# Kernel tuning notes

Hardware: AMD Instinct MI355X
Metric: run time of the kernel (lower is better)

## Reference

```python
import jax, jax.numpy as jnp
import numpy as np

N, E, G = 100_000, 1_600_000, 64
NODE_DIM, EDGE_DIM = 64, 16
H, C = 4, 16            # heads, per-head channels (hidden_dim=64)
HID = H * C             # 64
OUT = 128
NEG_SLOPE = 0.2


def _gatv2(x, src, dst, ea, Wl, bl, Wr, br, We, att, bias, n):
    """One GATv2Conv layer (PyG semantics, concat=True). src/dst include self-loops."""
    xl = (x @ Wl + bl).reshape(-1, H, C)   # [n,H,C] source transform
    xr = (x @ Wr + br).reshape(-1, H, C)   # [n,H,C] target transform
    e = (ea @ We).reshape(-1, H, C)        # [E2,H,C] edge transform (no bias)
    m = jax.nn.leaky_relu(xl[src] + xr[dst] + e, NEG_SLOPE)  # [E2,H,C]
    score = jnp.einsum('ehc,hc->eh', m, att)                 # [E2,H]
    smax = jax.ops.segment_max(score, dst, num_segments=n)   # scatter-softmax over dst
    z = jnp.exp(score - smax[dst])
    denom = jax.ops.segment_sum(z, dst, num_segments=n)
    alpha = z / denom[dst]                                   # [E2,H]
    out = jax.ops.segment_sum(alpha[..., None] * xl[src], dst, num_segments=n)
    return out.reshape(n, HID) + bias


def setup_inputs() -> dict:
    key = jax.random.key(0)
    ks = jax.random.split(key, 24)
    inp = {
        'node_features': jax.random.normal(ks[0], (N, NODE_DIM), jnp.float32),
        'edge_index': jax.random.randint(ks[1], (2, E), 0, N),
        'edge_attr': jax.random.normal(ks[2], (E, EDGE_DIM), jnp.float32),
        'batch': jnp.sort(jax.random.randint(ks[3], (N,), 0, G)),
    }
    s = 0.1
    i = 4
    for l, ind in (('l0', NODE_DIM), ('l1', HID)):
        inp[f'{l}_Wl'] = jax.random.normal(ks[i], (ind, HID), jnp.float32) * s; i += 1
        inp[f'{l}_bl'] = jnp.zeros((HID,), jnp.float32)
        inp[f'{l}_Wr'] = jax.random.normal(ks[i], (ind, HID), jnp.float32) * s; i += 1
        inp[f'{l}_br'] = jnp.zeros((HID,), jnp.float32)
        inp[f'{l}_We'] = jax.random.normal(ks[i], (EDGE_DIM, HID), jnp.float32) * s; i += 1
        inp[f'{l}_att'] = jax.random.normal(ks[i], (H, C), jnp.float32) * s; i += 1
        inp[f'{l}_bias'] = jnp.zeros((HID,), jnp.float32)
    inp['mlp_W1'] = jax.random.normal(ks[i], (HID, OUT), jnp.float32) * s; i += 1
    inp['mlp_b1'] = jnp.zeros((OUT,), jnp.float32)
    inp['mlp_W2'] = jax.random.normal(ks[i], (OUT, OUT), jnp.float32) * s
    inp['mlp_b2'] = jnp.zeros((OUT,), jnp.float32)
    return inp


def reference(node_features, edge_index, edge_attr, batch,
              l0_Wl, l0_bl, l0_Wr, l0_br, l0_We, l0_att, l0_bias,
              l1_Wl, l1_bl, l1_Wr, l1_br, l1_We, l1_att, l1_bias,
              mlp_W1, mlp_b1, mlp_W2, mlp_b2):
    n = node_features.shape[0]
    src, dst = edge_index[0], edge_index[1]
    # add_self_loops with fill_value='mean': self-loop attr = mean of incoming edge attrs
    cnt = jax.ops.segment_sum(jnp.ones((edge_attr.shape[0],), edge_attr.dtype), dst, num_segments=n)
    loop_attr = jax.ops.segment_sum(edge_attr, dst, num_segments=n) / jnp.maximum(cnt, 1.0)[:, None]
    loop = jnp.arange(n)
    src2 = jnp.concatenate([src, loop])
    dst2 = jnp.concatenate([dst, loop])
    ea2 = jnp.concatenate([edge_attr, loop_attr], axis=0)

    x = jax.nn.relu(_gatv2(node_features, src2, dst2, ea2,
                           l0_Wl, l0_bl, l0_Wr, l0_br, l0_We, l0_att, l0_bias, n))
    x = jax.nn.relu(_gatv2(x, src2, dst2, ea2,
                           l1_Wl, l1_bl, l1_Wr, l1_br, l1_We, l1_att, l1_bias, n))

    # global_mean_pool
    gcnt = jax.ops.segment_sum(jnp.ones((n,), x.dtype), batch, num_segments=G)
    g = jax.ops.segment_sum(x, batch, num_segments=G) / jnp.maximum(gcnt, 1.0)[:, None]

    return jax.nn.relu(g @ mlp_W1 + mlp_b1) @ mlp_W2 + mlp_b2
```

## Files before the change

### kernel.cpp

```cpp
#include <hip/hip_runtime.h>
#include <math.h>

#define HID 64
#define NH 4
#define NC 16
#define EDIM 16
#define OUTD 128
#define NEG 0.2f

typedef float v4f __attribute__((ext_vector_type(4)));
typedef float v2f __attribute__((ext_vector_type(2)));

__device__ __forceinline__ v2f pkfma(v2f a, v2f b, v2f c) {
    return __builtin_elementwise_fma(a, b, c);
}

template <int CTRL>
__device__ __forceinline__ float dpp_add(float x) {
    int t = __builtin_amdgcn_update_dpp(0, __float_as_int(x), CTRL, 0xF, 0xF, true);
    return x + __int_as_float(t);
}
__device__ __forceinline__ float red16(float x) {
    x = dpp_add<0xB1>(x);
    x = dpp_add<0x4E>(x);
    x = dpp_add<0x124>(x);
    x = dpp_add<0x128>(x);
    return x;
}



__global__ void hist_kernel(const int* __restrict__ dst, int* __restrict__ deg, int E) {
    int e = blockIdx.x * 256 + threadIdx.x;
    if (e < E) atomicAdd(&deg[dst[e]], 1);
}

__global__ void scan_a(const int* __restrict__ deg, int* __restrict__ offs,
                       int* __restrict__ bsum, int n) {
    __shared__ int tmp[1024];
    int i = blockIdx.x * 1024 + threadIdx.x;
    int v = (i < n) ? (deg[i] + 1) : 0;
    tmp[threadIdx.x] = v;
    __syncthreads();
    for (int off = 1; off < 1024; off <<= 1) {
        int t = (threadIdx.x >= off) ? tmp[threadIdx.x - off] : 0;
        __syncthreads();
        tmp[threadIdx.x] += t;
        __syncthreads();
    }
    if (i < n) offs[i] = tmp[threadIdx.x] - v;
    if (threadIdx.x == 1023) bsum[blockIdx.x] = tmp[1023];
}

__global__ void scan_b(int* __restrict__ bsum, int* __restrict__ offs, int nb, int n) {
    __shared__ int tmp[1024];
    int v = (threadIdx.x < nb) ? bsum[threadIdx.x] : 0;
    tmp[threadIdx.x] = v;
    __syncthreads();
    for (int off = 1; off < 1024; off <<= 1) {
        int t = (threadIdx.x >= off) ? tmp[threadIdx.x - off] : 0;
        __syncthreads();
        tmp[threadIdx.x] += t;
        __syncthreads();
    }
    if (threadIdx.x < nb) bsum[threadIdx.x] = tmp[threadIdx.x] - v;
    if (threadIdx.x == 1023) offs[n] = tmp[1023];
}

__global__ void scan_c(int* __restrict__ offs, const int* __restrict__ bsum, int n) {
    int i = blockIdx.x * 1024 + threadIdx.x;
    if (i < n) offs[i] += bsum[blockIdx.x];
}

__global__ void scatter_kernel(const int* __restrict__ src, const int* __restrict__ dst,
                               const v4f* __restrict__ ea,
                               const int* __restrict__ offs, int* __restrict__ cursor,
                               int* __restrict__ csr_src, v4f* __restrict__ csr_ea,
                               int E) {
    int e = blockIdx.x * 256 + threadIdx.x;
    if (e >= E) return;
    int d = dst[e];
    int p = offs[d] + 1 + atomicAdd(&cursor[d], 1);
    csr_src[p] = src[e];
    v4f a0 = ea[e * 4 + 0], a1 = ea[e * 4 + 1],
        a2 = ea[e * 4 + 2], a3 = ea[e * 4 + 3];
    csr_ea[p * 4 + 0] = a0;
    csr_ea[p * 4 + 1] = a1;
    csr_ea[p * 4 + 2] = a2;
    csr_ea[p * 4 + 3] = a3;
}

__global__ void loopattr_kernel(const int* __restrict__ offs, int* __restrict__ csr_src,
                                float* __restrict__ csr_ea_f, int n) {
    int idx = blockIdx.x * 256 + threadIdx.x;
    if (idx >= n * EDIM) return;
    int nd = idx >> 4, k = idx & 15;
    int e0 = offs[nd], e1 = offs[nd + 1];
    int deg = e1 - e0 - 1;
    float s = 0.f;
    for (int j = e0 + 1; j < e1; j++) s += csr_ea_f[(size_t)j * EDIM + k];
    csr_ea_f[(size_t)e0 * EDIM + k] = s / fmaxf((float)deg, 1.0f);
    if (k == 0) csr_src[e0] = nd;
}


__global__ __launch_bounds__(256)
void dualgemm_kernel(const float* __restrict__ x,
                     const float* __restrict__ Wl, const float* __restrict__ bl,
                     const float* __restrict__ Wr, const float* __restrict__ br,
                     float* __restrict__ xl, float* __restrict__ xr, int n) {
    __shared__ float xs[64 * 65];
    __shared__ float ws[64 * 128];
    int tid = threadIdx.x;
    int r0 = blockIdx.x * 64;

#pragma unroll
    for (int t = 0; t < 32; t++) {
        int idx = t * 256 + tid;
        int k = idx >> 7, j = idx & 127;
        ws[idx] = (j < 64) ? Wl[k * 64 + j] : Wr[k * 64 + (j - 64)];
    }
#pragma unroll
    for (int t = 0; t < 16; t++) {
        int idx = t * 256 + tid;
        int r = idx >> 6, c = idx & 63;
        float v = (r0 + r < n) ? x[(r0 + r) * 64 + c] : 0.f;
        xs[r * 65 + c] = v;
    }
    __syncthreads();

    int cg = tid & 31;
    int rg = tid >> 5;

    float acc[8][4];
#pragma unroll
    for (int u = 0; u < 8; u++)
#pragma unroll
        for (int v = 0; v < 4; v++) acc[u][v] = 0.f;

    for (int k = 0; k < 64; k++) {
        float4 wv = *(const float4*)&ws[k * 128 + cg * 4];
        float xv[8];
#pragma unroll
        for (int u = 0; u < 8; u++) xv[u] = xs[(rg * 8 + u) * 65 + k];
#pragma unroll
        for (int u = 0; u < 8; u++) {
            acc[u][0] += xv[u] * wv.x;
            acc[u][1] += xv[u] * wv.y;
            acc[u][2] += xv[u] * wv.z;
            acc[u][3] += xv[u] * wv.w;
        }
    }

    int j0 = cg * 4;
    bool isL = (j0 < 64);
    const float* bp = isL ? bl : br;
    float* op = isL ? xl : xr;
    int jj = isL ? j0 : (j0 - 64);
    float4 bv = *(const float4*)&bp[jj];
#pragma unroll
    for (int u = 0; u < 8; u++) {
        int r = r0 + rg * 8 + u;
        if (r < n) {
            float4 o;
            o.x = acc[u][0] + bv.x; o.y = acc[u][1] + bv.y;
            o.z = acc[u][2] + bv.z; o.w = acc[u][3] + bv.w;
            *(float4*)&op[r * 64 + jj] = o;
        }
    }
}


#define EDOT(A0, A1, A2, A3, INIT)                                         \
    ({ v2f _a = {(INIT), 0.f};                                             \
       _a = pkfma((v2f){A0.x, A0.y}, wec2[0], _a);                         \
       _a = pkfma((v2f){A0.z, A0.w}, wec2[1], _a);                         \
       _a = pkfma((v2f){A1.x, A1.y}, wec2[2], _a);                         \
       _a = pkfma((v2f){A1.z, A1.w}, wec2[3], _a);                         \
       _a = pkfma((v2f){A2.x, A2.y}, wec2[4], _a);                         \
       _a = pkfma((v2f){A2.z, A2.w}, wec2[5], _a);                         \
       _a = pkfma((v2f){A3.x, A3.y}, wec2[6], _a);                         \
       _a = pkfma((v2f){A3.z, A3.w}, wec2[7], _a);                         \
       _a.x + _a.y; })

__global__ __launch_bounds__(256)
void gat_kernel(const int* __restrict__ offs, const int* __restrict__ csr_src,
                const float4* __restrict__ csr_ea,
                const float* __restrict__ xl, const float* __restrict__ xr,
                const float* __restrict__ We, const float* __restrict__ att,
                const float* __restrict__ bias, float* __restrict__ out, int n) {
    int lane = threadIdx.x & 63;
    int node = __builtin_amdgcn_readfirstlane(blockIdx.x * 4 + (threadIdx.x >> 6));
    if (node >= n) return;

    v2f wec2[8];
#pragma unroll
    for (int k = 0; k < 8; k++) {
        wec2[k].x = We[(2 * k) * 64 + lane];
        wec2[k].y = We[(2 * k + 1) * 64 + lane];
    }
    const float LOG2E = 1.4426950408889634f;
    float attl = att[lane] * LOG2E;
    float xrl = xr[(size_t)node * 64 + lane];

    int e0 = __builtin_amdgcn_readfirstlane(offs[node]);
    int e1 = __builtin_amdgcn_readfirstlane(offs[node + 1]);

    float S = 0.f, acc = 0.f;
    int i = e0;

    if ((e1 - e0) & 1) {
        int s0 = csr_src[i];
        float4 A0 = csr_ea[i*4+0], A1 = csr_ea[i*4+1],
               A2 = csr_ea[i*4+2], A3 = csr_ea[i*4+3];
        float x0 = (xl + (size_t)s0 * 64)[lane];
        float m0 = EDOT(A0, A1, A2, A3, x0 + xrl);
        m0 = fmaxf(m0, NEG * m0);
        float p0 = red16(m0 * attl);
        float z0 = __builtin_amdgcn_exp2f(p0);
        S = z0; acc = z0 * x0;
        i++;
    }

    if (i < e1) {
        int sa = csr_src[i], sb = csr_src[i + 1];
        float4 A0 = csr_ea[i*4+0], A1 = csr_ea[i*4+1],
               A2 = csr_ea[i*4+2], A3 = csr_ea[i*4+3];
        float4 B0 = csr_ea[i*4+4], B1 = csr_ea[i*4+5],
               B2 = csr_ea[i*4+6], B3 = csr_ea[i*4+7];
        float xa = (xl + (size_t)sa * 64)[lane];
        float xb = (xl + (size_t)sb * 64)[lane];
        int last = e1 - 2;
        for (;;) {
            int j = i + 2;
            j = (j > last) ? last : j;
            int sa_n = csr_src[j], sb_n = csr_src[j + 1];
            float4 A0n = csr_ea[j*4+0], A1n = csr_ea[j*4+1],
                   A2n = csr_ea[j*4+2], A3n = csr_ea[j*4+3];
            float4 B0n = csr_ea[j*4+4], B1n = csr_ea[j*4+5],
                   B2n = csr_ea[j*4+6], B3n = csr_ea[j*4+7];
            float xa_n = (xl + (size_t)sa_n * 64)[lane];
            float xb_n = (xl + (size_t)sb_n * 64)[lane];

            float m0 = EDOT(A0, A1, A2, A3, xa + xrl);
            float m1 = EDOT(B0, B1, B2, B3, xb + xrl);
            m0 = fmaxf(m0, NEG * m0);
            m1 = fmaxf(m1, NEG * m1);
            float p0 = red16(m0 * attl);
            float p1 = red16(m1 * attl);
            float z0 = __builtin_amdgcn_exp2f(p0);
            float z1 = __builtin_amdgcn_exp2f(p1);
            S += z0 + z1;
            acc = fmaf(z0, xa, fmaf(z1, xb, acc));

            if (i >= last) break;
            i = j;
            sa = sa_n; sb = sb_n;
            A0 = A0n; A1 = A1n; A2 = A2n; A3 = A3n;
            B0 = B0n; B1 = B1n; B2 = B2n; B3 = B3n;
            xa = xa_n; xb = xb_n;
        }
    }
    out[(size_t)node * 64 + lane] = fmaxf(acc / S + bias[lane], 0.f);
}


__global__ __launch_bounds__(256)
void pool_mlp_kernel(const float* __restrict__ x, const int* __restrict__ batch, int n,
                     const float* __restrict__ W1, const float* __restrict__ b1,
                     const float* __restrict__ W2, const float* __restrict__ b2,
                     float* __restrict__ out) {
    __shared__ float psum[4][64];
    __shared__ float gv[64];
    __shared__ float hid[128];
    __shared__ int bounds[2];

    int g = blockIdx.x;
    int tid = threadIdx.x;
    int wave = tid >> 6, lane = tid & 63;

    if (tid < 2) {
        int target = g + tid;
        int lo = 0, hi = n;
        while (lo < hi) {
            int mid = (lo + hi) >> 1;
            if (batch[mid] < target) lo = mid + 1; else hi = mid;
        }
        bounds[tid] = lo;
    }
    __syncthreads();
    int lo = bounds[0], hi = bounds[1];
    int cnt = hi - lo;

    float s = 0.f;
    for (int nd = lo + wave; nd < hi; nd += 4)
        s += x[(size_t)nd * 64 + lane];
    psum[wave][lane] = s;
    __syncthreads();

    if (tid < 64)
        gv[tid] = (psum[0][tid] + psum[1][tid] + psum[2][tid] + psum[3][tid])
                  / fmaxf((float)cnt, 1.0f);
    __syncthreads();

    if (tid < 128) {
        float h = b1[tid];
        for (int k = 0; k < 64; k++) h += gv[k] * W1[k * 128 + tid];
        hid[tid] = fmaxf(h, 0.f);
    }
    __syncthreads();
    if (tid < 128) {
        float o = b2[tid];
        for (int k = 0; k < 128; k++) o += hid[k] * W2[k * 128 + tid];
        out[g * 128 + tid] = o;
    }
}


extern "C" void kernel_launch(void* const* d_in, const int* in_sizes, int n_in,
                              void* d_out, int out_size, void* d_ws, size_t ws_size,
                              hipStream_t stream) {
    const float* nf   = (const float*)d_in[0];
    const int*   ei   = (const int*)d_in[1];
    const float* eaw  = (const float*)d_in[2];
    const int*   bat  = (const int*)d_in[3];
    const float* l0_Wl = (const float*)d_in[4];
    const float* l0_bl = (const float*)d_in[5];
    const float* l0_Wr = (const float*)d_in[6];
    const float* l0_br = (const float*)d_in[7];
    const float* l0_We = (const float*)d_in[8];
    const float* l0_att = (const float*)d_in[9];
    const float* l0_bias = (const float*)d_in[10];
    const float* l1_Wl = (const float*)d_in[11];
    const float* l1_bl = (const float*)d_in[12];
    const float* l1_Wr = (const float*)d_in[13];
    const float* l1_br = (const float*)d_in[14];
    const float* l1_We = (const float*)d_in[15];
    const float* l1_att = (const float*)d_in[16];
    const float* l1_bias = (const float*)d_in[17];
    const float* mW1 = (const float*)d_in[18];
    const float* mb1 = (const float*)d_in[19];
    const float* mW2 = (const float*)d_in[20];
    const float* mb2 = (const float*)d_in[21];

    const int N = in_sizes[0] / 64;
    const int E = in_sizes[1] / 2;
    const int G = out_size / OUTD;

    char* w = (char*)d_ws;
    auto carve = [&](size_t bytes) {
        void* p = (void*)w;
        w += (bytes + 255) & ~(size_t)255;
        return p;
    };
    int*    deg     = (int*)carve((size_t)N * 4);
    int*    offs    = (int*)carve((size_t)(N + 1) * 4);
    int*    cursor  = (int*)carve((size_t)N * 4);
    int*    bsum    = (int*)carve(4096 * 4);
    int*    csr_src = (int*)carve((size_t)(E + N) * 4);
    v4f*    csr_ea  = (v4f*)carve((size_t)(E + N) * 64);
    float*  xl      = (float*)carve((size_t)N * 64 * 4);
    float*  xr      = (float*)carve((size_t)N * 64 * 4);
    float*  x1      = (float*)carve((size_t)N * 64 * 4);

    hipMemsetAsync(deg, 0, (size_t)N * 4, stream);
    hipMemsetAsync(cursor, 0, (size_t)N * 4, stream);

    const int* src = ei;
    const int* dst = ei + E;

    hist_kernel<<<(E + 255) / 256, 256, 0, stream>>>(dst, deg, E);

    int nb = (N + 1023) / 1024;
    scan_a<<<nb, 1024, 0, stream>>>(deg, offs, bsum, N);
    scan_b<<<1, 1024, 0, stream>>>(bsum, offs, nb, N);
    scan_c<<<nb, 1024, 0, stream>>>(offs, bsum, N);

    scatter_kernel<<<(E + 255) / 256, 256, 0, stream>>>(src, dst, (const v4f*)eaw,
                                                        offs, cursor, csr_src, csr_ea, E);
    loopattr_kernel<<<(N * EDIM + 255) / 256, 256, 0, stream>>>(offs, csr_src,
                                                                (float*)csr_ea, N);

    dualgemm_kernel<<<(N + 63) / 64, 256, 0, stream>>>(nf, l0_Wl, l0_bl, l0_Wr, l0_br,
                                                       xl, xr, N);
    gat_kernel<<<(N + 3) / 4, 256, 0, stream>>>(offs, csr_src, (const float4*)csr_ea,
                                                xl, xr, l0_We, l0_att, l0_bias, x1, N);
    dualgemm_kernel<<<(N + 63) / 64, 256, 0, stream>>>(x1, l1_Wl, l1_bl, l1_Wr, l1_br,
                                                       xl, xr, N);
    gat_kernel<<<(N + 3) / 4, 256, 0, stream>>>(offs, csr_src, (const float4*)csr_ea,
                                                xl, xr, l1_We, l1_att, l1_bias, x1, N);

    pool_mlp_kernel<<<G, 256, 0, stream>>>(x1, bat, N, mW1, mb1, mW2, mb2, (float*)d_out);
}
```

Baseline: 831.3 us.

## Reuse histogram atomic ranks in scatter and deepen GAT edge-load pipeline

The histogram kernel now stores each edge's atomicAdd return value as its rank, so the scatter kernel places edges without a second round of atomics or a cursor memset. The GAT edge loop becomes a three-stage rotating software pipeline: it loads source indices three pairs ahead, edge attributes two ahead and xl gathers one ahead, so more memory latency is hidden. This costs extra registers, which may reduce occupancy, and adds an E-sized rank buffer written and read once.

Result: faster. 803.6 us (-3.3%).

```diff
diff --git a/kernel.cpp b/kernel.cpp
--- a/kernel.cpp
+++ b/kernel.cpp
@@ -30,9 +30,10 @@
 
 
 
-__global__ void hist_kernel(const int* __restrict__ dst, int* __restrict__ deg, int E) {
+__global__ void hist_kernel(const int* __restrict__ dst, int* __restrict__ deg,
+                            int* __restrict__ rank, int E) {
     int e = blockIdx.x * 256 + threadIdx.x;
-    if (e < E) atomicAdd(&deg[dst[e]], 1);
+    if (e < E) rank[e] = atomicAdd(&deg[dst[e]], 1);
 }
 
 __global__ void scan_a(const int* __restrict__ deg, int* __restrict__ offs,
@@ -73,14 +74,15 @@
 }
 
 __global__ void scatter_kernel(const int* __restrict__ src, const int* __restrict__ dst,
+                               const int* __restrict__ rank,
                                const v4f* __restrict__ ea,
-                               const int* __restrict__ offs, int* __restrict__ cursor,
+                               const int* __restrict__ offs,
                                int* __restrict__ csr_src, v4f* __restrict__ csr_ea,
                                int E) {
     int e = blockIdx.x * 256 + threadIdx.x;
     if (e >= E) return;
     int d = dst[e];
-    int p = offs[d] + 1 + atomicAdd(&cursor[d], 1);
+    int p = offs[d] + 1 + rank[e];
     csr_src[p] = src[e];
     v4f a0 = ea[e * 4 + 0], a1 = ea[e * 4 + 1],
         a2 = ea[e * 4 + 2], a3 = ea[e * 4 + 3];
@@ -183,6 +185,35 @@
        _a = pkfma((v2f){A3.z, A3.w}, wec2[7], _a);                         \
        _a.x + _a.y; })
 
+#define LOADS(K, BI) do { int _s = base + 2 * (K);                         \
+    sb##BI##0 = csr_src[_s]; sb##BI##1 = csr_src[_s + 1]; } while (0)
+#define LOADA(K, BI) do { int _q = (base + 2 * (K)) * 4;                   \
+    ab##BI##0 = csr_ea[_q + 0]; ab##BI##1 = csr_ea[_q + 1];                \
+    ab##BI##2 = csr_ea[_q + 2]; ab##BI##3 = csr_ea[_q + 3];                \
+    ab##BI##4 = csr_ea[_q + 4]; ab##BI##5 = csr_ea[_q + 5];                \
+    ab##BI##6 = csr_ea[_q + 6]; ab##BI##7 = csr_ea[_q + 7]; } while (0)
+#define GATH(BI) do {                                                      \
+    xa##BI = (xl + (size_t)sb##BI##0 * 64)[lane];                          \
+    xc##BI = (xl + (size_t)sb##BI##1 * 64)[lane]; } while (0)
+#define COMP(BI) do {                                                      \
+    float m0 = EDOT(ab##BI##0, ab##BI##1, ab##BI##2, ab##BI##3, xa##BI + xrl); \
+    float m1 = EDOT(ab##BI##4, ab##BI##5, ab##BI##6, ab##BI##7, xc##BI + xrl); \
+    m0 = fmaxf(m0, NEG * m0);                                              \
+    m1 = fmaxf(m1, NEG * m1);                                              \
+    float p0 = red16(m0 * attl);                                           \
+    float p1 = red16(m1 * attl);                                           \
+    float z0 = __builtin_amdgcn_exp2f(p0);                                 \
+    float z1 = __builtin_amdgcn_exp2f(p1);                                 \
+    S += z0 + z1;                                                          \
+    acc = fmaf(z0, xa##BI, fmaf(z1, xc##BI, acc)); } while (0)
+#define PHASE(P, Q) do {                                                   \
+    int _k2 = t + 2; _k2 = (_k2 > lastp) ? lastp : _k2;                    \
+    int _k3 = t + 3; _k3 = (_k3 > lastp) ? lastp : _k3;                    \
+    GATH(Q);                                                               \
+    LOADA(_k2, Q);                                                         \
+    LOADS(_k3, P);                                                         \
+    COMP(P); } while (0)
+
 __global__ __launch_bounds__(256)
 void gat_kernel(const int* __restrict__ offs, const int* __restrict__ csr_src,
                 const float4* __restrict__ csr_ea,
@@ -223,42 +254,25 @@
     }
 
     if (i < e1) {
-        int sa = csr_src[i], sb = csr_src[i + 1];
-        float4 A0 = csr_ea[i*4+0], A1 = csr_ea[i*4+1],
-               A2 = csr_ea[i*4+2], A3 = csr_ea[i*4+3];
-        float4 B0 = csr_ea[i*4+4], B1 = csr_ea[i*4+5],
-               B2 = csr_ea[i*4+6], B3 = csr_ea[i*4+7];
-        float xa = (xl + (size_t)sa * 64)[lane];
-        float xb = (xl + (size_t)sb * 64)[lane];
-        int last = e1 - 2;
+        int base = i;
+        int lastp = ((e1 - i) >> 1) - 1;
+        int sb00, sb01, sb10, sb11, sb20, sb21;
+        float4 ab00, ab01, ab02, ab03, ab04, ab05, ab06, ab07;
+        float4 ab10, ab11, ab12, ab13, ab14, ab15, ab16, ab17;
+        float4 ab20, ab21, ab22, ab23, ab24, ab25, ab26, ab27;
+        float xa0, xc0, xa1, xc1, xa2, xc2;
+
+        int k1 = (1 > lastp) ? lastp : 1;
+        int k2 = (2 > lastp) ? lastp : 2;
+        LOADS(0, 0); LOADS(k1, 1); LOADS(k2, 2);
+        LOADA(0, 0); LOADA(k1, 1);
+        GATH(0); GATH(1);
+
+        int t = 0;
         for (;;) {
-            int j = i + 2;
-            j = (j > last) ? last : j;
-            int sa_n = csr_src[j], sb_n = csr_src[j + 1];
-            float4 A0n = csr_ea[j*4+0], A1n = csr_ea[j*4+1],
-                   A2n = csr_ea[j*4+2], A3n = csr_ea[j*4+3];
-            float4 B0n = csr_ea[j*4+4], B1n = csr_ea[j*4+5],
-                   B2n = csr_ea[j*4+6], B3n = csr_ea[j*4+7];
-            float xa_n = (xl + (size_t)sa_n * 64)[lane];
-            float xb_n = (xl + (size_t)sb_n * 64)[lane];
-
-            float m0 = EDOT(A0, A1, A2, A3, xa + xrl);
-            float m1 = EDOT(B0, B1, B2, B3, xb + xrl);
-            m0 = fmaxf(m0, NEG * m0);
-            m1 = fmaxf(m1, NEG * m1);
-            float p0 = red16(m0 * attl);
-            float p1 = red16(m1 * attl);
-            float z0 = __builtin_amdgcn_exp2f(p0);
-            float z1 = __builtin_amdgcn_exp2f(p1);
-            S += z0 + z1;
-            acc = fmaf(z0, xa, fmaf(z1, xb, acc));
-
-            if (i >= last) break;
-            i = j;
-            sa = sa_n; sb = sb_n;
-            A0 = A0n; A1 = A1n; A2 = A2n; A3 = A3n;
-            B0 = B0n; B1 = B1n; B2 = B2n; B3 = B3n;
-            xa = xa_n; xb = xb_n;
+            PHASE(0, 2); if (t >= lastp) break; ++t;
+            PHASE(1, 0); if (t >= lastp) break; ++t;
+            PHASE(2, 1); if (t >= lastp) break; ++t;
         }
     }
     out[(size_t)node * 64 + lane] = fmaxf(acc / S + bias[lane], 0.f);
@@ -355,7 +369,7 @@
     };
     int*    deg     = (int*)carve((size_t)N * 4);
     int*    offs    = (int*)carve((size_t)(N + 1) * 4);
-    int*    cursor  = (int*)carve((size_t)N * 4);
+    int*    rank    = (int*)carve((size_t)E * 4);
     int*    bsum    = (int*)carve(4096 * 4);
     int*    csr_src = (int*)carve((size_t)(E + N) * 4);
     v4f*    csr_ea  = (v4f*)carve((size_t)(E + N) * 64);
@@ -364,20 +378,19 @@
     float*  x1      = (float*)carve((size_t)N * 64 * 4);
 
     hipMemsetAsync(deg, 0, (size_t)N * 4, stream);
-    hipMemsetAsync(cursor, 0, (size_t)N * 4, stream);
 
     const int* src = ei;
     const int* dst = ei + E;
 
-    hist_kernel<<<(E + 255) / 256, 256, 0, stream>>>(dst, deg, E);
+    hist_kernel<<<(E + 255) / 256, 256, 0, stream>>>(dst, deg, rank, E);
 
     int nb = (N + 1023) / 1024;
     scan_a<<<nb, 1024, 0, stream>>>(deg, offs, bsum, N);
     scan_b<<<1, 1024, 0, stream>>>(bsum, offs, nb, N);
     scan_c<<<nb, 1024, 0, stream>>>(offs, bsum, N);
 
-    scatter_kernel<<<(E + 255) / 256, 256, 0, stream>>>(src, dst, (const v4f*)eaw,
-                                                        offs, cursor, csr_src, csr_ea, E);
+    scatter_kernel<<<(E + 255) / 256, 256, 0, stream>>>(src, dst, rank, (const v4f*)eaw,
+                                                        offs, csr_src, csr_ea, E);
     loopattr_kernel<<<(N * EDIM + 255) / 256, 256, 0, stream>>>(offs, csr_src,
                                                                 (float*)csr_ea, N);
 
```
